# Kernel optimization log

Hardware: AMD Instinct MI355X
Metric: run time of the kernel (lower is better)

## Reference

```python
import jax, jax.numpy as jnp
import numpy as np

D, DK, DV = 1024, 128, 128
N = 8192


def setup_inputs() -> dict:
    key = jax.random.key(0)
    ks = jax.random.split(key, 7)
    s = 1.0 / np.sqrt(D)
    return {
        "X": jax.random.normal(ks[0], (N, D), dtype=jnp.float32),
        "Wq": jax.random.uniform(ks[1], (D, DK), jnp.float32, -s, s),
        "bq": jax.random.uniform(ks[2], (DK,), jnp.float32, -s, s),
        "Wk": jax.random.uniform(ks[3], (D, DK), jnp.float32, -s, s),
        "bk": jax.random.uniform(ks[4], (DK,), jnp.float32, -s, s),
        "Wv": jax.random.uniform(ks[5], (D, DV), jnp.float32, -s, s),
        "bv": jax.random.uniform(ks[6], (DV,), jnp.float32, -s, s),
    }


def reference(X, Wq, bq, Wk, bk, Wv, bv):
    # Projections (torch Linear: y = x @ W^T + b; here W stored as [in, out])
    Q = X @ Wq + bq            # [N, d_k]
    K = X @ Wk + bk            # [N, d_k]
    V = X @ Wv + bv            # [N, d_v]
    n, d_k = Q.shape
    scores = (Q @ K.T) / jnp.sqrt(jnp.asarray(d_k, Q.dtype))  # [N, N]
    # Causal mask: positions j > i get -inf before softmax
    causal = jnp.tril(jnp.ones((n, n), dtype=bool))
    scores = jnp.where(causal, scores, -jnp.inf)
    weights = jax.nn.softmax(scores, axis=-1)  # [N, N]
    return weights @ V          # [N, d_v]
```

## Files before the change

kernel.cpp:

```cpp
#include <hip/hip_runtime.h>
#include <hip/hip_bf16.h>

#define N_TOK 8192
#define D_IN  1024
#define DK    128
#define NT    256

typedef __attribute__((ext_vector_type(8))) short short8;
typedef __attribute__((ext_vector_type(4))) float f32x4;

static __device__ __forceinline__ unsigned short f2bf(float f) {
    __hip_bfloat16 h = __float2bfloat16(f);
    return __builtin_bit_cast(unsigned short, h);
}

static __device__ __forceinline__ void gl_lds16(const void* g, void* l) {
    __builtin_amdgcn_global_load_lds(
        (const __attribute__((address_space(1))) void*)g,
        (__attribute__((address_space(3))) void*)l, 16, 0, 0);
}

__global__ __launch_bounds__(256) void wtrans_kernel(
    const float* __restrict__ Wq, const float* __restrict__ Wk,
    const float* __restrict__ Wv, unsigned short* __restrict__ Wt)
{
    __shared__ unsigned short T[64][72];
    const int proj = blockIdx.y;
    const float* W = (proj == 0) ? Wq : (proj == 1) ? Wk : Wv;
    unsigned short* out = Wt + (size_t)proj * DK * D_IN;
    const int k0 = (blockIdx.x & 15) * 64, n0 = (blockIdx.x >> 4) * 64;
    const int tid = threadIdx.x;
    #pragma unroll
    for (int i = 0; i < 4; i++) {
        int e = tid + i * 256;
        int r = e >> 4, c4 = e & 15;
        float4 v = *reinterpret_cast<const float4*>(&W[(size_t)(k0 + r) * DK + n0 + c4 * 4]);
        T[c4 * 4 + 0][r] = f2bf(v.x);
        T[c4 * 4 + 1][r] = f2bf(v.y);
        T[c4 * 4 + 2][r] = f2bf(v.z);
        T[c4 * 4 + 3][r] = f2bf(v.w);
    }
    __syncthreads();
    #pragma unroll
    for (int i = 0; i < 4; i++) {
        int e = tid + i * 256;
        int r = e >> 4, c4 = e & 15;
        *reinterpret_cast<ushort4*>(&out[(size_t)(n0 + r) * D_IN + k0 + c4 * 4]) =
            *reinterpret_cast<const ushort4*>(&T[r][c4 * 4]);
    }
}

__global__ __launch_bounds__(256) void xcast_kernel(
    const float* __restrict__ X, unsigned short* __restrict__ Xb)
{
    const int idx = blockIdx.x * 256 + threadIdx.x;
    const int m = idx >> 7, b = idx & 127;
    const float* src = &X[(size_t)m * D_IN + b * 8];
    const float4 v0 = *reinterpret_cast<const float4*>(src);
    const float4 v1 = *reinterpret_cast<const float4*>(src + 4);
    short8 h;
    h[0] = f2bf(v0.x); h[1] = f2bf(v0.y); h[2] = f2bf(v0.z); h[3] = f2bf(v0.w);
    h[4] = f2bf(v1.x); h[5] = f2bf(v1.y); h[6] = f2bf(v1.z); h[7] = f2bf(v1.w);
    const int bp = (b & ~7) | ((b & 7) ^ (m & 7));
    *reinterpret_cast<short8*>(&Xb[(size_t)m * D_IN + bp * 8]) = h;
}

__global__ __launch_bounds__(256, 2) void proj_fused(
    const unsigned short* __restrict__ Xb, const unsigned short* __restrict__ Wt,
    const float* __restrict__ bq, const float* __restrict__ bk,
    const float* __restrict__ bv,
    unsigned short* __restrict__ Qb, unsigned short* __restrict__ Kb,
    unsigned short* __restrict__ Vt)
{
    __shared__ unsigned short Xs[2][64][64];

    const int bid = blockIdx.x;
    const int t2 = bid >> 3;
    const int rb = (t2 / 6) * 8 + (bid & 7);
    const int cg = t2 % 6;

    const int tid = threadIdx.x;
    const int wid = tid >> 6, lane = tid & 63;
    const int g = lane >> 4, r16 = lane & 15;
    const int mb = rb * 64;
    const int colv = cg * 64 + wid * 16 + r16;
    const int pj = colv >> 7;
    const int n  = colv & 127;

    short8 wf[32];
    #pragma unroll
    for (int kd = 0; kd < 32; kd++)
        wf[kd] = *reinterpret_cast<const short8*>(
            &Wt[((size_t)pj * DK + n) * D_IN + kd * 32 + g * 8]);

    f32x4 acc[4] = {};

    auto STAGE_X = [&](int buf, int s) {
        #pragma unroll
        for (int i = 0; i < 2; i++) {
            int off = i * 4096 + tid * 16;
            int r = off >> 7, cb = off & 127;
            gl_lds16((const char*)Xb + (((size_t)(mb + r) * D_IN + s * 64) << 1) + cb,
                     (char*)&Xs[buf][0][0] + off);
        }
    };

    STAGE_X(0, 0);
    #pragma unroll
    for (int s = 0; s < 16; ++s) {
        const int cur = s & 1;
        if (s + 1 < 16) {
            STAGE_X(cur ^ 1, s + 1);
            asm volatile("s_waitcnt vmcnt(2)" ::: "memory");
        } else {
            asm volatile("s_waitcnt vmcnt(0)" ::: "memory");
        }
        __builtin_amdgcn_sched_barrier(0);
        __builtin_amdgcn_s_barrier();
        __builtin_amdgcn_sched_barrier(0);

        #pragma unroll
        for (int kk = 0; kk < 2; kk++) {
            short8 af[4];
            #pragma unroll
            for (int mi = 0; mi < 4; mi++) {
                int blk = ((kk << 2) | g) ^ (r16 & 7);
                af[mi] = *reinterpret_cast<const short8*>(
                    &Xs[cur][mi * 16 + r16][blk * 8]);
            }
            __builtin_amdgcn_s_setprio(1);
            #pragma unroll
            for (int mi = 0; mi < 4; mi++)
                acc[mi] = __builtin_amdgcn_mfma_f32_16x16x32_bf16(
                    af[mi], wf[2 * s + kk], acc[mi], 0, 0, 0);
            __builtin_amdgcn_s_setprio(0);
        }
        __builtin_amdgcn_sched_barrier(0);
        __builtin_amdgcn_s_barrier();
        __builtin_amdgcn_sched_barrier(0);
    }

    const float* bias = (pj == 0) ? bq : (pj == 1) ? bk : bv;
    float b = bias[n];
    #pragma unroll
    for (int mi = 0; mi < 4; mi++) {
        if (pj < 2) {
            unsigned short* out = (pj == 0) ? Qb : Kb;
            #pragma unroll
            for (int e = 0; e < 4; e++) {
                int m = mb + mi * 16 + g * 4 + e;
                float val = acc[mi][e] + b;
                int nc = n;
                if (pj == 1)
                    nc = ((((n >> 3) ^ (m & 7)) << 3) | (n & 7));
                out[(size_t)m * DK + nc] = f2bf(val);
            }
        } else {
            int m0 = mb + mi * 16 + g * 4;
            int mblk = (((m0 & 31) >> 3) ^ (n & 3));
            int mp = (m0 & ~31) | (mblk << 3) | (m0 & 7);
            ushort4 h;
            h.x = f2bf(acc[mi][0] + b);
            h.y = f2bf(acc[mi][1] + b);
            h.z = f2bf(acc[mi][2] + b);
            h.w = f2bf(acc[mi][3] + b);
            *reinterpret_cast<ushort4*>(&Vt[(size_t)n * N_TOK + mp]) = h;
        }
    }
}

__global__ __launch_bounds__(256, 3) void attn_partial(
    const unsigned short* __restrict__ Qb, const unsigned short* __restrict__ Ksw,
    const unsigned short* __restrict__ Vsw,
    unsigned short* __restrict__ OpartH, float* __restrict__ Mpart,
    float* __restrict__ Lpart,
    float* __restrict__ O, int chunk_tiles, int max_chunks, int direct)
{
    __shared__ unsigned short Klds[2][32][128];
    __shared__ unsigned short Vlds[2][128][32];
    __shared__ unsigned short Pq[4][32][36];

    const int qb = blockIdx.x, c = blockIdx.y;
    const int j0 = c * chunk_tiles;
    const int jmax = 4 * qb + 4;
    const int jend = min(j0 + chunk_tiles, jmax);
    if (j0 >= jend) return;
    const int nt = jend - j0;

    const int tid = threadIdx.x;
    const int wid = tid >> 6, lane = tid & 63;
    const int g = lane >> 4, r16 = lane & 15;
    const int t = qb * 4 + wid;
    const int qw = t * 32;
    const float scale2 = 0.08838834764831845f * 1.4426950408889634f;

    auto STAGE = [&](int buf, int kvb) {
        #pragma unroll
        for (int s = 0; s < 2; s++) {
            int ob = ((wid * 2 + s) << 10);
            gl_lds16((const char*)Ksw + ((size_t)kvb << 8) + ob + (lane << 4),
                     (char*)&Klds[buf][0][0] + ob);
        }
        #pragma unroll
        for (int s = 0; s < 2; s++) {
            int ob = ((wid * 2 + s) << 10);
            int o = ob + (lane << 4);
            int d = o >> 6, cb = o & 63;
            gl_lds16((const char*)Vsw + (((size_t)d * N_TOK + kvb) << 1) + cb,
                     (char*)&Vlds[buf][0][0] + ob);
        }
    };

    short8 qf[2][4];
    #pragma unroll
    for (int mi = 0; mi < 2; mi++)
        #pragma unroll
        for (int kd = 0; kd < 4; kd++)
            qf[mi][kd] = *reinterpret_cast<const short8*>(
                &Qb[(size_t)(qw + mi * 16 + r16) * DK + kd * 32 + g * 8]);

    f32x4 o_acc[2][8] = {};
    float m_run[2] = {-1e30f, -1e30f}, l_run[2] = {0.f, 0.f};

    STAGE(0, j0 * 32);

    int cur = 0;
    for (int it = 0; it < nt; ++it) {
        const int kvb = (j0 + it) * 32;
        if (it + 1 < nt) {
            STAGE(cur ^ 1, kvb + 32);
            asm volatile("s_waitcnt vmcnt(4)" ::: "memory");
        } else {
            asm volatile("s_waitcnt vmcnt(0)" ::: "memory");
        }
        __builtin_amdgcn_sched_barrier(0);
        __builtin_amdgcn_s_barrier();
        __builtin_amdgcn_sched_barrier(0);

        const unsigned short* Kl = &Klds[cur][0][0];
        const unsigned short* Vl = &Vlds[cur][0][0];

        f32x4 st[2][2] = {};
        #pragma unroll
        for (int kd = 0; kd < 4; kd++) {
            int swb = ((((kd << 2) | g) ^ (r16 & 7)) << 3);
            short8 kf0 = *reinterpret_cast<const short8*>(Kl + r16 * 128 + swb);
            short8 kf1 = *reinterpret_cast<const short8*>(Kl + (16 + r16) * 128 + swb);
            __builtin_amdgcn_s_setprio(1);
            st[0][0] = __builtin_amdgcn_mfma_f32_16x16x32_bf16(kf0, qf[0][kd], st[0][0], 0, 0, 0);
            st[0][1] = __builtin_amdgcn_mfma_f32_16x16x32_bf16(kf0, qf[1][kd], st[0][1], 0, 0, 0);
            st[1][0] = __builtin_amdgcn_mfma_f32_16x16x32_bf16(kf1, qf[0][kd], st[1][0], 0, 0, 0);
            st[1][1] = __builtin_amdgcn_mfma_f32_16x16x32_bf16(kf1, qf[1][kd], st[1][1], 0, 0, 0);
            __builtin_amdgcn_s_setprio(0);
        }

        const bool anymask = (kvb + 31 > qw);
        float alpha[2];
        #pragma unroll
        for (int mi = 0; mi < 2; mi++) {
            const int qrow = qw + mi * 16 + r16;
            float s[2][4];
            #pragma unroll
            for (int ni = 0; ni < 2; ni++)
                #pragma unroll
                for (int e = 0; e < 4; e++) {
                    float v = st[ni][mi][e] * scale2;
                    if (anymask && (kvb + ni * 16 + g * 4 + e > qrow)) v = -1e30f;
                    s[ni][e] = v;
                }
            float lm = fmaxf(fmaxf(fmaxf(s[0][0], s[0][1]), fmaxf(s[0][2], s[0][3])),
                             fmaxf(fmaxf(s[1][0], s[1][1]), fmaxf(s[1][2], s[1][3])));
            lm = fmaxf(lm, __shfl_xor(lm, 16));
            lm = fmaxf(lm, __shfl_xor(lm, 32));
            float mnew = fmaxf(m_run[mi], lm);
            alpha[mi] = exp2f(m_run[mi] - mnew);
            float ps[2][4];
            #pragma unroll
            for (int ni = 0; ni < 2; ni++)
                #pragma unroll
                for (int e = 0; e < 4; e++)
                    ps[ni][e] = exp2f(s[ni][e] - mnew);
            float ls = ((ps[0][0] + ps[0][1]) + (ps[0][2] + ps[0][3]))
                     + ((ps[1][0] + ps[1][1]) + (ps[1][2] + ps[1][3]));
            ls += __shfl_xor(ls, 16);
            ls += __shfl_xor(ls, 32);
            l_run[mi] = l_run[mi] * alpha[mi] + ls;
            m_run[mi] = mnew;
            #pragma unroll
            for (int ni = 0; ni < 2; ni++) {
                ushort4 pk;
                pk.x = f2bf(ps[ni][0]); pk.y = f2bf(ps[ni][1]);
                pk.z = f2bf(ps[ni][2]); pk.w = f2bf(ps[ni][3]);
                *reinterpret_cast<ushort4*>(&Pq[wid][mi * 16 + r16][ni * 16 + g * 4]) = pk;
            }
        }
        if (__any(alpha[0] < 1.f) || __any(alpha[1] < 1.f)) {
            #pragma unroll
            for (int mi = 0; mi < 2; mi++)
                #pragma unroll
                for (int df = 0; df < 8; df++)
                    #pragma unroll
                    for (int e = 0; e < 4; e++)
                        o_acc[mi][df][e] *= alpha[mi];
        }
        short8 pb0 = *reinterpret_cast<const short8*>(&Pq[wid][r16][g * 8]);
        short8 pb1 = *reinterpret_cast<const short8*>(&Pq[wid][16 + r16][g * 8]);
        const int swv = ((g ^ (r16 & 3)) << 3);
        #pragma unroll
        for (int df = 0; df < 8; df++) {
            short8 vf = *reinterpret_cast<const short8*>(Vl + (df * 16 + r16) * 32 + swv);
            __builtin_amdgcn_s_setprio(1);
            o_acc[0][df] = __builtin_amdgcn_mfma_f32_16x16x32_bf16(vf, pb0, o_acc[0][df], 0, 0, 0);
            o_acc[1][df] = __builtin_amdgcn_mfma_f32_16x16x32_bf16(vf, pb1, o_acc[1][df], 0, 0, 0);
            __builtin_amdgcn_s_setprio(0);
        }

        __builtin_amdgcn_sched_barrier(0);
        __builtin_amdgcn_s_barrier();
        __builtin_amdgcn_sched_barrier(0);
        cur ^= 1;
    }

    if (direct) {
        #pragma unroll
        for (int mi = 0; mi < 2; mi++) {
            float inv = 1.0f / l_run[mi];
            #pragma unroll
            for (int df = 0; df < 8; df++) {
                f32x4 r = o_acc[mi][df];
                r[0] *= inv; r[1] *= inv; r[2] *= inv; r[3] *= inv;
                *reinterpret_cast<f32x4*>(
                    &O[(size_t)(qw + mi * 16 + r16) * DK + df * 16 + g * 4]) = r;
            }
        }
    } else {
        size_t pb0i = ((size_t)t * max_chunks + c) * 32;
        #pragma unroll
        for (int mi = 0; mi < 2; mi++) {
            int q = mi * 16 + r16;
            #pragma unroll
            for (int df = 0; df < 8; df++) {
                ushort4 h;
                h.x = f2bf(o_acc[mi][df][0]); h.y = f2bf(o_acc[mi][df][1]);
                h.z = f2bf(o_acc[mi][df][2]); h.w = f2bf(o_acc[mi][df][3]);
                *reinterpret_cast<ushort4*>(
                    &OpartH[(pb0i + q) * 128 + df * 16 + g * 4]) = h;
            }
            if (g == 0) { Mpart[pb0i + q] = m_run[mi]; Lpart[pb0i + q] = l_run[mi]; }
        }
    }
}

__global__ __launch_bounds__(256) void attn_merge(
    const unsigned short* __restrict__ OpartH, const float* __restrict__ Mpart,
    const float* __restrict__ Lpart, float* __restrict__ O,
    int chunk_tiles, int max_chunks)
{
    __shared__ float Ms[32], Ls[32], Fs[16][32];
    const int t = blockIdx.x;
    const int nc = t / chunk_tiles + 1;
    const int tid = threadIdx.x;

    if (tid < 32) {
        float M = -1e30f;
        for (int c = 0; c < nc; c++)
            M = fmaxf(M, Mpart[((size_t)t * max_chunks + c) * 32 + tid]);
        float L = 0.f;
        for (int c = 0; c < nc; c++) {
            size_t pb = ((size_t)t * max_chunks + c) * 32 + tid;
            L += exp2f(Mpart[pb] - M) * Lpart[pb];
        }
        Ms[tid] = M; Ls[tid] = L;
    }
    __syncthreads();
    for (int cc = tid >> 5; cc < nc; cc += 8) {
        int row = tid & 31;
        Fs[cc][row] = exp2f(Mpart[((size_t)t * max_chunks + cc) * 32 + row] - Ms[row]);
    }
    __syncthreads();
    #pragma unroll
    for (int it = 0; it < 2; it++) {
        int idx = tid + it * 256;
        int row = idx >> 4, c8 = idx & 15;
        float accv[8] = {};
        for (int c = 0; c < nc; c++) {
            short8 u = *reinterpret_cast<const short8*>(
                &OpartH[(((size_t)t * max_chunks + c) * 32 + row) * 128 + c8 * 8]);
            float f = Fs[c][row];
            #pragma unroll
            for (int k = 0; k < 8; k++) {
                unsigned uv = ((unsigned)(unsigned short)u[k]) << 16;
                accv[k] += f * __builtin_bit_cast(float, uv);
            }
        }
        float inv = 1.0f / Ls[row];
        float* dst = &O[((size_t)t * 32 + row) * DK + c8 * 8];
        float4 r0 = {accv[0] * inv, accv[1] * inv, accv[2] * inv, accv[3] * inv};
        float4 r1 = {accv[4] * inv, accv[5] * inv, accv[6] * inv, accv[7] * inv};
        *reinterpret_cast<float4*>(dst) = r0;
        *reinterpret_cast<float4*>(dst + 4) = r1;
    }
}

extern "C" void kernel_launch(void* const* d_in, const int* in_sizes, int n_in,
                              void* d_out, int out_size, void* d_ws, size_t ws_size,
                              hipStream_t stream) {
    const float* X  = (const float*)d_in[0];
    const float* Wq = (const float*)d_in[1];
    const float* bq = (const float*)d_in[2];
    const float* Wk = (const float*)d_in[3];
    const float* bk = (const float*)d_in[4];
    const float* Wv = (const float*)d_in[5];
    const float* bv = (const float*)d_in[6];
    float* O = (float*)d_out;

    unsigned short* Qb = (unsigned short*)d_ws;
    unsigned short* Kb = Qb + (size_t)N_TOK * DK;
    unsigned short* Vt = Kb + (size_t)N_TOK * DK;
    unsigned short* Wt = Vt + (size_t)N_TOK * DK;
    unsigned short* Xb = Wt + (size_t)3 * DK * D_IN;
    float* Mbase = (float*)(Xb + (size_t)N_TOK * D_IN);
    size_t base_bytes = (size_t)((char*)Mbase - (char*)d_ws);

    int chunk_tiles = 0, max_chunks = 1, direct = 0;
    const int opts[4] = {16, 32, 64, 128};
    for (int i = 0; i < 4; i++) {
        int ct = opts[i], mc = NT / ct;
        size_t need = base_bytes
                    + (size_t)NT * mc * 32 * 2 * sizeof(float)
                    + (size_t)NT * mc * 32 * 128 * 2;
        if (need <= ws_size) { chunk_tiles = ct; max_chunks = mc; break; }
    }
    if (!chunk_tiles) { chunk_tiles = NT; max_chunks = 1; direct = 1; }
    float* Mpart = Mbase;
    float* Lpart = Mpart + (size_t)NT * max_chunks * 32;
    unsigned short* OpartH = (unsigned short*)(Lpart + (size_t)NT * max_chunks * 32);

    wtrans_kernel<<<dim3(32, 3), 256, 0, stream>>>(Wq, Wk, Wv, Wt);
    xcast_kernel<<<dim3(4096), 256, 0, stream>>>(X, Xb);
    proj_fused<<<dim3(768), 256, 0, stream>>>(Xb, Wt, bq, bk, bv, Qb, Kb, Vt);
    int grid_c = direct ? 1 : max_chunks;
    attn_partial<<<dim3(64, grid_c), 256, 0, stream>>>(
        Qb, Kb, Vt, OpartH, Mpart, Lpart, O, chunk_tiles, max_chunks, direct);
    if (!direct)
        attn_merge<<<dim3(NT), 256, 0, stream>>>(OpartH, Mpart, Lpart, O,
                                                 chunk_tiles, max_chunks);
}
```

Before: 101.8 us.

## Fuse X bf16 cast into projection kernel and split merge across two blocks

Drops the separate xcast kernel. The projection kernel now loads fp32 X straight into registers, converts it to bf16 and writes it to swizzled LDS, with the next stage's loads overlapping the current MFMAs. This removes a full 8192x1024 bf16 round-trip through global memory and one launch. The cost is that X fp32 is now read six times (once per column group) instead of bf16, and the async global-to-LDS path is replaced by register staging. Separately, the merge kernel runs two blocks per tile, each handling half of the columns, to raise parallelism.

New measurement: 99.62 us. 2.2% less time.

```diff
diff --git a/kernel.cpp b/kernel.cpp
--- a/kernel.cpp
+++ b/kernel.cpp
@@ -50,23 +50,8 @@
     }
 }
 
-__global__ __launch_bounds__(256) void xcast_kernel(
-    const float* __restrict__ X, unsigned short* __restrict__ Xb)
-{
-    const int idx = blockIdx.x * 256 + threadIdx.x;
-    const int m = idx >> 7, b = idx & 127;
-    const float* src = &X[(size_t)m * D_IN + b * 8];
-    const float4 v0 = *reinterpret_cast<const float4*>(src);
-    const float4 v1 = *reinterpret_cast<const float4*>(src + 4);
-    short8 h;
-    h[0] = f2bf(v0.x); h[1] = f2bf(v0.y); h[2] = f2bf(v0.z); h[3] = f2bf(v0.w);
-    h[4] = f2bf(v1.x); h[5] = f2bf(v1.y); h[6] = f2bf(v1.z); h[7] = f2bf(v1.w);
-    const int bp = (b & ~7) | ((b & 7) ^ (m & 7));
-    *reinterpret_cast<short8*>(&Xb[(size_t)m * D_IN + bp * 8]) = h;
-}
-
 __global__ __launch_bounds__(256, 2) void proj_fused(
-    const unsigned short* __restrict__ Xb, const unsigned short* __restrict__ Wt,
+    const float* __restrict__ X, const unsigned short* __restrict__ Wt,
     const float* __restrict__ bq, const float* __restrict__ bk,
     const float* __restrict__ bv,
     unsigned short* __restrict__ Qb, unsigned short* __restrict__ Kb,
@@ -95,30 +80,35 @@
 
     f32x4 acc[4] = {};
 
-    auto STAGE_X = [&](int buf, int s) {
-        #pragma unroll
-        for (int i = 0; i < 2; i++) {
-            int off = i * 4096 + tid * 16;
-            int r = off >> 7, cb = off & 127;
-            gl_lds16((const char*)Xb + (((size_t)(mb + r) * D_IN + s * 64) << 1) + cb,
-                     (char*)&Xs[buf][0][0] + off);
+    float4 xr[4];
+    const int xr_r  = tid >> 4;
+    const int xr_c4 = tid & 15;
+    auto XLOAD = [&](int s) {
+        #pragma unroll
+        for (int i = 0; i < 4; i++) {
+            int r = (tid + i * 256) >> 4;
+            xr[i] = *reinterpret_cast<const float4*>(
+                &X[(size_t)(mb + r) * D_IN + s * 64 + xr_c4 * 4]);
         }
     };
-
-    STAGE_X(0, 0);
+    auto XWRITE = [&](int buf) {
+        #pragma unroll
+        for (int i = 0; i < 4; i++) {
+            int r = (tid + i * 256) >> 4;
+            ushort4 h;
+            h.x = f2bf(xr[i].x); h.y = f2bf(xr[i].y);
+            h.z = f2bf(xr[i].z); h.w = f2bf(xr[i].w);
+            int off = (((xr_c4 >> 1) ^ (r & 7)) << 3) | ((xr_c4 & 1) << 2);
+            *reinterpret_cast<ushort4*>(&Xs[buf][r][off]) = h;
+        }
+    };
+
+    XLOAD(0); XWRITE(0);
+    __syncthreads();
     #pragma unroll
     for (int s = 0; s < 16; ++s) {
         const int cur = s & 1;
-        if (s + 1 < 16) {
-            STAGE_X(cur ^ 1, s + 1);
-            asm volatile("s_waitcnt vmcnt(2)" ::: "memory");
-        } else {
-            asm volatile("s_waitcnt vmcnt(0)" ::: "memory");
-        }
-        __builtin_amdgcn_sched_barrier(0);
-        __builtin_amdgcn_s_barrier();
-        __builtin_amdgcn_sched_barrier(0);
-
+        if (s + 1 < 16) XLOAD(s + 1);
         #pragma unroll
         for (int kk = 0; kk < 2; kk++) {
             short8 af[4];
@@ -135,9 +125,8 @@
                     af[mi], wf[2 * s + kk], acc[mi], 0, 0, 0);
             __builtin_amdgcn_s_setprio(0);
         }
-        __builtin_amdgcn_sched_barrier(0);
-        __builtin_amdgcn_s_barrier();
-        __builtin_amdgcn_sched_barrier(0);
+        if (s + 1 < 16) XWRITE((s + 1) & 1);
+        __syncthreads();
     }
 
     const float* bias = (pj == 0) ? bq : (pj == 1) ? bk : bv;
@@ -358,6 +347,7 @@
 {
     __shared__ float Ms[32], Ls[32], Fs[16][32];
     const int t = blockIdx.x;
+    const int half = blockIdx.y;
     const int nc = t / chunk_tiles + 1;
     const int tid = threadIdx.x;
 
@@ -378,10 +368,9 @@
         Fs[cc][row] = exp2f(Mpart[((size_t)t * max_chunks + cc) * 32 + row] - Ms[row]);
     }
     __syncthreads();
-    #pragma unroll
-    for (int it = 0; it < 2; it++) {
-        int idx = tid + it * 256;
-        int row = idx >> 4, c8 = idx & 15;
+    {
+        int row = tid >> 3;
+        int c8 = (tid & 7) + half * 8;
         float accv[8] = {};
         for (int c = 0; c < nc; c++) {
             short8 u = *reinterpret_cast<const short8*>(
@@ -418,8 +407,7 @@
     unsigned short* Kb = Qb + (size_t)N_TOK * DK;
     unsigned short* Vt = Kb + (size_t)N_TOK * DK;
     unsigned short* Wt = Vt + (size_t)N_TOK * DK;
-    unsigned short* Xb = Wt + (size_t)3 * DK * D_IN;
-    float* Mbase = (float*)(Xb + (size_t)N_TOK * D_IN);
+    float* Mbase = (float*)(Wt + (size_t)3 * DK * D_IN);
     size_t base_bytes = (size_t)((char*)Mbase - (char*)d_ws);
 
     int chunk_tiles = 0, max_chunks = 1, direct = 0;
@@ -437,12 +425,11 @@
     unsigned short* OpartH = (unsigned short*)(Lpart + (size_t)NT * max_chunks * 32);
 
     wtrans_kernel<<<dim3(32, 3), 256, 0, stream>>>(Wq, Wk, Wv, Wt);
-    xcast_kernel<<<dim3(4096), 256, 0, stream>>>(X, Xb);
-    proj_fused<<<dim3(768), 256, 0, stream>>>(Xb, Wt, bq, bk, bv, Qb, Kb, Vt);
+    proj_fused<<<dim3(768), 256, 0, stream>>>(X, Wt, bq, bk, bv, Qb, Kb, Vt);
     int grid_c = direct ? 1 : max_chunks;
     attn_partial<<<dim3(64, grid_c), 256, 0, stream>>>(
         Qb, Kb, Vt, OpartH, Mpart, Lpart, O, chunk_tiles, max_chunks, direct);
     if (!direct)
-        attn_merge<<<dim3(NT), 256, 0, stream>>>(OpartH, Mpart, Lpart, O,
-                                                 chunk_tiles, max_chunks);
-}
+        attn_merge<<<dim3(NT, 2), 256, 0, stream>>>(OpartH, Mpart, Lpart, O,
+                                                    chunk_tiles, max_chunks);
+}
```
